# Kernel tuning notes

Measured on AMD Instinct MI355X. Metric: run time of the kernel, lower is better.

## Reference

```python
import jax, jax.numpy as jnp
import numpy as np

B, NQ, NK = 128, 64, 64
D_Q_IN = D_K_IN = D_V_IN = 1024
H, DK, DV = 16, 64, 64
D_OUT = 1024
TEMP = float(np.power(DK, 0.5))


def setup_inputs() -> dict:
    key = jax.random.key(0)
    ks = jax.random.split(key, 10)
    s = 0.01  # GroupLinearLayer init scale (0.01 * randn)
    return {
        "q": jax.random.normal(ks[0], (B, NQ, D_Q_IN), jnp.float32),
        "k": jax.random.normal(ks[1], (B, NK, D_K_IN), jnp.float32),
        "v": jax.random.normal(ks[2], (B, NK, D_V_IN), jnp.float32),
        "w_q": s * jax.random.normal(ks[3], (NQ, D_Q_IN, H * DK), jnp.float32),
        "w_k": s * jax.random.normal(ks[4], (NK, D_K_IN, H * DK), jnp.float32),
        "w_v": s * jax.random.normal(ks[5], (NK, D_V_IN, H * DV), jnp.float32),
        "fc_w": jax.random.normal(ks[6], (D_OUT, H * DV), jnp.float32) / np.sqrt(H * DV),
        "fc_b": jnp.zeros((D_OUT,), jnp.float32),
        "gate_w": jax.random.normal(ks[7], (D_OUT, H * DV), jnp.float32) / np.sqrt(H * DV),
        "gate_b": jnp.zeros((D_OUT,), jnp.float32),
    }


def reference(q, k, v, w_q, w_k, w_v, fc_w, fc_b, gate_w, gate_b):
    # Grouped (per-position) linear projections: weight [n, d_in, H*dh]
    qp = jnp.einsum('bnd,nde->bne', q, w_q).reshape(B, NQ, H, DK)
    kp = jnp.einsum('bnd,nde->bne', k, w_k).reshape(B, NK, H, DK)
    vp = jnp.einsum('bnd,nde->bne', v, w_v).reshape(B, NK, H, DV)
    # scaled dot-product attention per head
    scores = jnp.einsum('bqhd,bkhd->bhqk', qp, kp) / TEMP
    attn = jax.nn.softmax(scores, axis=-1)          # [B,H,NQ,NK]
    out = jnp.einsum('bhqk,bkhd->bqhd', attn, vp)   # [B,NQ,H,DV]
    out = out.reshape(B, NQ, H * DV)
    # fc + gated tanh output (residual=True branch; dropout p=0 -> identity)
    fc_out = out @ fc_w.T + fc_b
    gate = jax.nn.sigmoid(out @ gate_w.T + gate_b)
    output = gate * jnp.tanh(fc_out)
    return (output, attn)
```

## Files before the change

kernel.cpp:

```cpp
#include <hip/hip_runtime.h>

#define B_    128
#define NPOS  64
#define DIN   1024
#define HH    16
#define DH    64
#define E_    1024

typedef __bf16 bf16x8 __attribute__((ext_vector_type(8)));
typedef float  f32x4  __attribute__((ext_vector_type(4)));

union F4 { float4 v; float f[4]; };

__device__ __forceinline__ unsigned int pk2bf(float a, float b) {
    unsigned int ua = __float_as_uint(a);
    unsigned int ub = __float_as_uint(b);
    ua = (ua + 0x7fffu + ((ua >> 16) & 1u)) >> 16;
    ub = (ub + 0x7fffu + ((ub >> 16) & 1u)) >> 16;
    return ua | (ub << 16);
}
__device__ __forceinline__ unsigned short f2bf(float a) {
    unsigned int u = __float_as_uint(a);
    u = (u + 0x7fffu + ((u >> 16) & 1u)) >> 16;
    return (unsigned short)u;
}
__device__ __forceinline__ float bf2f(unsigned int u) {
    return __uint_as_float(u << 16);
}

__global__ __launch_bounds__(256, 3) void proj_kernel(
    const float* __restrict__ qin, const float* __restrict__ kin, const float* __restrict__ vin,
    const float* __restrict__ wq,  const float* __restrict__ wk,  const float* __restrict__ wv,
    unsigned short* __restrict__ qp, unsigned short* __restrict__ kp, unsigned short* __restrict__ vp) {
    const int e0 = blockIdx.x * 128;
    const int n  = blockIdx.y;
    const int z  = blockIdx.z;
    const float* in = (z == 0) ? qin : (z == 1) ? kin : vin;
    const float* w  = (z == 0) ? wq  : (z == 1) ? wk  : wv;
    unsigned short* outp = (z == 0) ? qp : (z == 1) ? kp : vp;

    __shared__ __attribute__((aligned(16))) unsigned short As[128 * 72];
    __shared__ __attribute__((aligned(16))) unsigned short Bs[128 * 72];

    const int t = threadIdx.x;
    const int lane = t & 63, wave = t >> 6;
    const int wm = wave >> 1, wn = wave & 1;

    f32x4 acc[4][4];
#pragma unroll
    for (int i = 0; i < 4; i++)
#pragma unroll
        for (int j = 0; j < 4; j++) acc[i][j] = (f32x4){0.f, 0.f, 0.f, 0.f};

    const float* inA = in + n * DIN;
    const float* wB  = w + (size_t)n * DIN * E_ + e0;

    const int afr = t & 15, ar0 = t >> 4;
    const int beb = t & 31, bkq = t >> 5;
    const int bS  = (beb & 7) << 4;

    F4 rA[8];
    F4 rB[2][4];

#pragma unroll
    for (int p = 0; p < 8; p++)
        rA[p].v = *(const float4*)(inA + (size_t)(ar0 + p * 16) * (NPOS * DIN) + afr * 4);
#pragma unroll
    for (int p = 0; p < 2; p++) {
        const float* src = wB + (size_t)((bkq + p * 8) * 4) * E_ + beb * 4;
#pragma unroll
        for (int x = 0; x < 4; x++) rB[p][x].v = *(const float4*)(src + (size_t)x * E_);
    }

    for (int kb = 0; kb < DIN; kb += 64) {
#pragma unroll
        for (int p = 0; p < 8; p++) {
            int row = ar0 + p * 16;
            uint2 pk; pk.x = pk2bf(rA[p].f[0], rA[p].f[1]); pk.y = pk2bf(rA[p].f[2], rA[p].f[3]);
            *(uint2*)&As[row * 72 + afr * 4] = pk;
        }
#pragma unroll
        for (int p = 0; p < 2; p++) {
            int kby = ((bkq + p * 8) * 8) ^ bS;
#pragma unroll
            for (int x = 0; x < 4; x++) {
                uint2 pk; pk.x = pk2bf(rB[p][0].f[x], rB[p][1].f[x]);
                pk.y = pk2bf(rB[p][2].f[x], rB[p][3].f[x]);
                *(uint2*)((char*)Bs + (beb * 4 + x) * 144 + kby) = pk;
            }
        }
        __syncthreads();
        if (kb + 64 < DIN) {
            const int kn = kb + 64;
#pragma unroll
            for (int p = 0; p < 8; p++)
                rA[p].v = *(const float4*)(inA + (size_t)(ar0 + p * 16) * (NPOS * DIN) + kn + afr * 4);
#pragma unroll
            for (int p = 0; p < 2; p++) {
                const float* src = wB + (size_t)(kn + (bkq + p * 8) * 4) * E_ + beb * 4;
#pragma unroll
                for (int x = 0; x < 4; x++) rB[p][x].v = *(const float4*)(src + (size_t)x * E_);
            }
        }
#pragma unroll
        for (int ks = 0; ks < 64; ks += 32) {
            bf16x8 a[4], b[4];
            const int koff = ks + (lane >> 4) * 8;
#pragma unroll
            for (int i = 0; i < 4; i++)
                a[i] = *(const bf16x8*)&As[(wm * 64 + i * 16 + (lane & 15)) * 72 + koff];
#pragma unroll
            for (int j = 0; j < 4; j++) {
                int row = wn * 64 + j * 16 + (lane & 15);
                b[j] = *(const bf16x8*)((const char*)Bs + row * 144 +
                                        ((2 * koff) ^ (((row >> 2) & 7) << 4)));
            }
#pragma unroll
            for (int i = 0; i < 4; i++)
#pragma unroll
                for (int j = 0; j < 4; j++)
                    acc[i][j] = __builtin_amdgcn_mfma_f32_16x16x32_bf16(a[i], b[j], acc[i][j], 0, 0, 0);
        }
        __syncthreads();
    }
    const int col_l = lane & 15, rq = lane >> 4;
#pragma unroll
    for (int i = 0; i < 4; i++)
#pragma unroll
        for (int j = 0; j < 4; j++) {
            int e = e0 + wn * 64 + j * 16 + col_l;
#pragma unroll
            for (int r = 0; r < 4; r++) {
                int m = wm * 64 + i * 16 + rq * 4 + r;
                outp[(size_t)m * (NPOS * E_) + n * E_ + e] = f2bf(acc[i][j][r]);
            }
        }
}

__global__ __launch_bounds__(256) void attn_kernel(
    const unsigned short* __restrict__ qp, const unsigned short* __restrict__ kp,
    const unsigned short* __restrict__ vp,
    float* __restrict__ attn_out,
    unsigned short* __restrict__ out_ws) {
    const int bid = blockIdx.x;
    const int b = bid >> 4, h = bid & 15;
    __shared__ __attribute__((aligned(16))) float qs[64 * 68];
    __shared__ __attribute__((aligned(16))) float kt[64 * 68];
    __shared__ __attribute__((aligned(16))) float sc[64 * 68];
    const int t = threadIdx.x;
    const size_t base = (size_t)b * 64 * E_ + h * DH;

#pragma unroll
    for (int p = 0; p < 4; p++) {
        int idx = p * 1024 + t * 4;
        int r = idx >> 6, c = idx & 63;
        uint2 q2 = *(const uint2*)(qp + base + r * E_ + c);
        float4 qv = { bf2f(q2.x & 0xffffu), bf2f(q2.x >> 16), bf2f(q2.y & 0xffffu), bf2f(q2.y >> 16) };
        *(float4*)&qs[r * 68 + c] = qv;
        uint2 k2 = *(const uint2*)(kp + base + r * E_ + c);
        kt[(c + 0) * 68 + r] = bf2f(k2.x & 0xffffu);
        kt[(c + 1) * 68 + r] = bf2f(k2.x >> 16);
        kt[(c + 2) * 68 + r] = bf2f(k2.y & 0xffffu);
        kt[(c + 3) * 68 + r] = bf2f(k2.y >> 16);
    }
    __syncthreads();
    const int ti = t >> 4, tj = t & 15;
    const int i0 = ti * 4, j0 = tj * 4;
    float s[4][4] = {};
    for (int k4 = 0; k4 < 64; k4 += 4) {
        F4 qv[4], kv[4];
#pragma unroll
        for (int r = 0; r < 4; r++) qv[r].v = *(const float4*)&qs[(i0 + r) * 68 + k4];
#pragma unroll
        for (int kk = 0; kk < 4; kk++) kv[kk].v = *(const float4*)&kt[(k4 + kk) * 68 + j0];
#pragma unroll
        for (int r = 0; r < 4; r++)
#pragma unroll
            for (int c = 0; c < 4; c++)
#pragma unroll
                for (int kk = 0; kk < 4; kk++)
                    s[r][c] += qv[r].f[kk] * kv[kk].f[c];
    }
#pragma unroll
    for (int r = 0; r < 4; r++)
#pragma unroll
        for (int c = 0; c < 4; c++)
            sc[(i0 + r) * 68 + j0 + c] = s[r][c] * 0.125f;
    __syncthreads();
#pragma unroll
    for (int p = 0; p < 4; p++) {
        int idx = p * 1024 + t * 4;
        int r = idx >> 6, c = idx & 63;
        uint2 v2 = *(const uint2*)(vp + base + r * E_ + c);
        float4 vv = { bf2f(v2.x & 0xffffu), bf2f(v2.x >> 16), bf2f(v2.y & 0xffffu), bf2f(v2.y >> 16) };
        *(float4*)&qs[r * 68 + c] = vv;
    }
    if (t < 64) {
        float m = -1e30f;
        for (int j = 0; j < 64; j++) m = fmaxf(m, sc[t * 68 + j]);
        float sum = 0.f;
        for (int j = 0; j < 64; j++) {
            float e = __expf(sc[t * 68 + j] - m);
            sc[t * 68 + j] = e; sum += e;
        }
        float inv = 1.f / sum;
        for (int j = 0; j < 64; j++) sc[t * 68 + j] *= inv;
    }
    __syncthreads();
    float* abase = attn_out + (size_t)bid * 4096;
#pragma unroll
    for (int p = 0; p < 4; p++) {
        int idx = p * 1024 + t * 4;
        int r = idx >> 6, c = idx & 63;
        float4 av = { sc[r * 68 + c], sc[r * 68 + c + 1], sc[r * 68 + c + 2], sc[r * 68 + c + 3] };
        *(float4*)(abase + idx) = av;
    }
    float o[4][4] = {};
    for (int j4 = 0; j4 < 64; j4 += 4) {
        F4 av[4], vv[4];
#pragma unroll
        for (int r = 0; r < 4; r++) av[r].v = *(const float4*)&sc[(i0 + r) * 68 + j4];
#pragma unroll
        for (int jj = 0; jj < 4; jj++) vv[jj].v = *(const float4*)&qs[(j4 + jj) * 68 + j0];
#pragma unroll
        for (int r = 0; r < 4; r++)
#pragma unroll
            for (int c = 0; c < 4; c++)
#pragma unroll
                for (int jj = 0; jj < 4; jj++)
                    o[r][c] += av[r].f[jj] * vv[jj].f[c];
    }
#pragma unroll
    for (int r = 0; r < 4; r++) {
        uint2 pk; pk.x = pk2bf(o[r][0], o[r][1]); pk.y = pk2bf(o[r][2], o[r][3]);
        *(uint2*)(out_ws + (size_t)(b * 64 + i0 + r) * E_ + h * DH + j0) = pk;
    }
}

__global__ __launch_bounds__(256, 2) void fcgate_kernel(
    const unsigned short* __restrict__ a,
    const float* __restrict__ fcw, const float* __restrict__ fcb,
    const float* __restrict__ gw,  const float* __restrict__ gb,
    float* __restrict__ outp) {
    const int n0 = blockIdx.x * 128;
    const int m0 = blockIdx.y * 128;
    __shared__ __attribute__((aligned(16))) unsigned short As[128 * 72];
    __shared__ __attribute__((aligned(16))) unsigned short Bf[128 * 72];
    __shared__ __attribute__((aligned(16))) unsigned short Bg[128 * 72];
    const int t = threadIdx.x;
    const int lane = t & 63, wave = t >> 6;
    const int wm = wave >> 1, wn = wave & 1;

    f32x4 accf[4][4], accg[4][4];
#pragma unroll
    for (int i = 0; i < 4; i++)
#pragma unroll
        for (int j = 0; j < 4; j++) {
            accf[i][j] = (f32x4){0.f, 0.f, 0.f, 0.f};
            accg[i][j] = (f32x4){0.f, 0.f, 0.f, 0.f};
        }

    const int afr = t & 7,  ar0 = t >> 3;
    const int bfr = t & 15, br0 = t >> 4;

    for (int kb = 0; kb < 1024; kb += 64) {
#pragma unroll
        for (int p = 0; p < 4; p++) {
            int row = ar0 + p * 32;
            *(uint4*)&As[row * 72 + afr * 8] =
                *(const uint4*)(a + (size_t)(m0 + row) * 1024 + kb + afr * 8);
        }
#pragma unroll
        for (int p = 0; p < 8; p++) {
            int row = br0 + p * 16;
            F4 cf; cf.v = *(const float4*)(fcw + (size_t)(n0 + row) * 1024 + kb + bfr * 4);
            uint2 pkf; pkf.x = pk2bf(cf.f[0], cf.f[1]); pkf.y = pk2bf(cf.f[2], cf.f[3]);
            *(uint2*)&Bf[row * 72 + bfr * 4] = pkf;
            F4 cg; cg.v = *(const float4*)(gw + (size_t)(n0 + row) * 1024 + kb + bfr * 4);
            uint2 pkg; pkg.x = pk2bf(cg.f[0], cg.f[1]); pkg.y = pk2bf(cg.f[2], cg.f[3]);
            *(uint2*)&Bg[row * 72 + bfr * 4] = pkg;
        }
        __syncthreads();
#pragma unroll
        for (int ks = 0; ks < 64; ks += 32) {
            bf16x8 av[4], bfv[4], bgv[4];
            const int koff = ks + (lane >> 4) * 8;
#pragma unroll
            for (int i = 0; i < 4; i++)
                av[i] = *(const bf16x8*)&As[(wm * 64 + i * 16 + (lane & 15)) * 72 + koff];
#pragma unroll
            for (int j = 0; j < 4; j++) {
                bfv[j] = *(const bf16x8*)&Bf[(wn * 64 + j * 16 + (lane & 15)) * 72 + koff];
                bgv[j] = *(const bf16x8*)&Bg[(wn * 64 + j * 16 + (lane & 15)) * 72 + koff];
            }
#pragma unroll
            for (int i = 0; i < 4; i++)
#pragma unroll
                for (int j = 0; j < 4; j++) {
                    accf[i][j] = __builtin_amdgcn_mfma_f32_16x16x32_bf16(av[i], bfv[j], accf[i][j], 0, 0, 0);
                    accg[i][j] = __builtin_amdgcn_mfma_f32_16x16x32_bf16(av[i], bgv[j], accg[i][j], 0, 0, 0);
                }
        }
        __syncthreads();
    }
    const int col_l = lane & 15, rq = lane >> 4;
#pragma unroll
    for (int i = 0; i < 4; i++)
#pragma unroll
        for (int j = 0; j < 4; j++) {
            int col = n0 + wn * 64 + j * 16 + col_l;
            float bfb = fcb[col], bgb = gb[col];
#pragma unroll
            for (int r = 0; r < 4; r++) {
                int m = m0 + wm * 64 + i * 16 + rq * 4 + r;
                float f = accf[i][j][r] + bfb;
                float g = accg[i][j][r] + bgb;
                float ef = __expf(2.f * f);
                float th = (ef - 1.f) / (ef + 1.f);
                float sg = 1.f / (1.f + __expf(-g));
                outp[(size_t)m * 1024 + col] = sg * th;
            }
        }
}

extern "C" void kernel_launch(void* const* d_in, const int* in_sizes, int n_in,
                              void* d_out, int out_size, void* d_ws, size_t ws_size,
                              hipStream_t stream) {
    const float* q      = (const float*)d_in[0];
    const float* k      = (const float*)d_in[1];
    const float* v      = (const float*)d_in[2];
    const float* w_q    = (const float*)d_in[3];
    const float* w_k    = (const float*)d_in[4];
    const float* w_v    = (const float*)d_in[5];
    const float* fc_w   = (const float*)d_in[6];
    const float* fc_b   = (const float*)d_in[7];
    const float* gate_w = (const float*)d_in[8];
    const float* gate_b = (const float*)d_in[9];

    float* out  = (float*)d_out;
    float* attn = out + 8388608;

    unsigned short* qp  = (unsigned short*)d_ws;
    unsigned short* kp  = qp + 8388608;
    unsigned short* vp  = kp + 8388608;
    unsigned short* ows = vp + 8388608;

    dim3 blk(256);
    proj_kernel<<<dim3(8, 64, 3), blk, 0, stream>>>(q, k, v, w_q, w_k, w_v, qp, kp, vp);
    attn_kernel<<<dim3(2048), blk, 0, stream>>>(qp, kp, vp, attn, ows);
    fcgate_kernel<<<dim3(8, 64), blk, 0, stream>>>(ows, fc_w, fc_b, gate_w, gate_b, out);
}
```

Baseline: 983.7 us.

## Rewrite attention kernel with bf16 MFMA and register-resident softmax

Replaces the scalar FP32 attention (QK^T, softmax, PV through shared-memory float tiles) with MFMA 16x16x32 bf16 instructions. Q and K fragments load straight from global memory, softmax runs in registers using lane shuffles, and V is stored transposed in swizzled LDS. The probabilities are split into hi/lo bf16 parts for two MFMAs to keep PV accuracy close to FP32. The projection kernel's B-tile swizzle pattern also changes to reduce LDS bank conflicts. The attn output is now written with scalar stores in the MFMA layout, which are less coalesced than the earlier float4 writes.

```diff
diff --git a/kernel.cpp b/kernel.cpp
--- a/kernel.cpp
+++ b/kernel.cpp
@@ -57,7 +57,7 @@
 
     const int afr = t & 15, ar0 = t >> 4;
     const int beb = t & 31, bkq = t >> 5;
-    const int bS  = (beb & 7) << 4;
+    const int bS  = ((beb >> 1) & 7) << 4;
 
     F4 rA[8];
     F4 rB[2][4];
@@ -113,7 +113,7 @@
             for (int j = 0; j < 4; j++) {
                 int row = wn * 64 + j * 16 + (lane & 15);
                 b[j] = *(const bf16x8*)((const char*)Bs + row * 144 +
-                                        ((2 * koff) ^ (((row >> 2) & 7) << 4)));
+                                        ((2 * koff) ^ (((row >> 3) & 7) << 4)));
             }
 #pragma unroll
             for (int i = 0; i < 4; i++)
@@ -144,97 +144,114 @@
     unsigned short* __restrict__ out_ws) {
     const int bid = blockIdx.x;
     const int b = bid >> 4, h = bid & 15;
-    __shared__ __attribute__((aligned(16))) float qs[64 * 68];
-    __shared__ __attribute__((aligned(16))) float kt[64 * 68];
-    __shared__ __attribute__((aligned(16))) float sc[64 * 68];
+    __shared__ __attribute__((aligned(16))) unsigned short Vt[64 * 72];
+    __shared__ __attribute__((aligned(16))) unsigned short P2[2][64 * 72];
     const int t = threadIdx.x;
-    const size_t base = (size_t)b * 64 * E_ + h * DH;
-
-#pragma unroll
-    for (int p = 0; p < 4; p++) {
-        int idx = p * 1024 + t * 4;
-        int r = idx >> 6, c = idx & 63;
-        uint2 q2 = *(const uint2*)(qp + base + r * E_ + c);
-        float4 qv = { bf2f(q2.x & 0xffffu), bf2f(q2.x >> 16), bf2f(q2.y & 0xffffu), bf2f(q2.y >> 16) };
-        *(float4*)&qs[r * 68 + c] = qv;
-        uint2 k2 = *(const uint2*)(kp + base + r * E_ + c);
-        kt[(c + 0) * 68 + r] = bf2f(k2.x & 0xffffu);
-        kt[(c + 1) * 68 + r] = bf2f(k2.x >> 16);
-        kt[(c + 2) * 68 + r] = bf2f(k2.y & 0xffffu);
-        kt[(c + 3) * 68 + r] = bf2f(k2.y >> 16);
-    }
+    const int lane = t & 63, w = t >> 6;
+    const int lr = lane & 15, lg = lane >> 4;
+    const size_t base = (size_t)b * (64 * E_) + h * DH;
+
+    const int d0 = (t & 15) * 4, j0 = (t >> 4) * 4;
+    union U2 { uint2 u; unsigned short s[4]; };
+    U2 L0, L1, L2, L3;
+    L0.u = *(const uint2*)(vp + base + (size_t)(j0 + 0) * E_ + d0);
+    L1.u = *(const uint2*)(vp + base + (size_t)(j0 + 1) * E_ + d0);
+    L2.u = *(const uint2*)(vp + base + (size_t)(j0 + 2) * E_ + d0);
+    L3.u = *(const uint2*)(vp + base + (size_t)(j0 + 3) * E_ + d0);
+
+    bf16x8 aq[2], bk[4][2];
+#pragma unroll
+    for (int ks = 0; ks < 2; ks++)
+        aq[ks] = *(const bf16x8*)(qp + base + (size_t)(w * 16 + lr) * E_ + ks * 32 + lg * 8);
+#pragma unroll
+    for (int jt = 0; jt < 4; jt++)
+#pragma unroll
+        for (int ks = 0; ks < 2; ks++)
+            bk[jt][ks] = *(const bf16x8*)(kp + base + (size_t)(jt * 16 + lr) * E_ + ks * 32 + lg * 8);
+
+#pragma unroll
+    for (int x = 0; x < 4; x++) {
+        U2 S; S.s[0] = L0.s[x]; S.s[1] = L1.s[x]; S.s[2] = L2.s[x]; S.s[3] = L3.s[x];
+        int row = d0 + x;
+        *(uint2*)((char*)Vt + row * 144 + ((j0 * 2) ^ (((row >> 3) & 7) << 4))) = S.u;
+    }
+
+    f32x4 s4[4];
+#pragma unroll
+    for (int jt = 0; jt < 4; jt++) s4[jt] = (f32x4){0.f, 0.f, 0.f, 0.f};
+#pragma unroll
+    for (int jt = 0; jt < 4; jt++)
+#pragma unroll
+        for (int ks = 0; ks < 2; ks++)
+            s4[jt] = __builtin_amdgcn_mfma_f32_16x16x32_bf16(aq[ks], bk[jt][ks], s4[jt], 0, 0, 0);
+
+    float p[4][4];
+#pragma unroll
+    for (int jt = 0; jt < 4; jt++)
+#pragma unroll
+        for (int r = 0; r < 4; r++) p[jt][r] = s4[jt][r] * 0.125f;
+
+#pragma unroll
+    for (int r = 0; r < 4; r++) {
+        float m = fmaxf(fmaxf(p[0][r], p[1][r]), fmaxf(p[2][r], p[3][r]));
+#pragma unroll
+        for (int msk = 1; msk < 16; msk <<= 1) m = fmaxf(m, __shfl_xor(m, msk));
+        float e0 = __expf(p[0][r] - m), e1 = __expf(p[1][r] - m);
+        float e2 = __expf(p[2][r] - m), e3 = __expf(p[3][r] - m);
+        float sum = (e0 + e1) + (e2 + e3);
+#pragma unroll
+        for (int msk = 1; msk < 16; msk <<= 1) sum += __shfl_xor(sum, msk);
+        float inv = 1.f / sum;
+        p[0][r] = e0 * inv; p[1][r] = e1 * inv; p[2][r] = e2 * inv; p[3][r] = e3 * inv;
+    }
+
+    float* abase = attn_out + (size_t)bid * 4096;
+#pragma unroll
+    for (int jt = 0; jt < 4; jt++)
+#pragma unroll
+        for (int r = 0; r < 4; r++) {
+            int q = w * 16 + lg * 4 + r;
+            abase[q * 64 + jt * 16 + lr] = p[jt][r];
+            unsigned short hs = f2bf(p[jt][r]);
+            float lo = p[jt][r] - bf2f(hs);
+            P2[0][q * 72 + jt * 16 + lr] = hs;
+            P2[1][q * 72 + jt * 16 + lr] = f2bf(lo);
+        }
     __syncthreads();
-    const int ti = t >> 4, tj = t & 15;
-    const int i0 = ti * 4, j0 = tj * 4;
-    float s[4][4] = {};
-    for (int k4 = 0; k4 < 64; k4 += 4) {
-        F4 qv[4], kv[4];
-#pragma unroll
-        for (int r = 0; r < 4; r++) qv[r].v = *(const float4*)&qs[(i0 + r) * 68 + k4];
-#pragma unroll
-        for (int kk = 0; kk < 4; kk++) kv[kk].v = *(const float4*)&kt[(k4 + kk) * 68 + j0];
-#pragma unroll
-        for (int r = 0; r < 4; r++)
-#pragma unroll
-            for (int c = 0; c < 4; c++)
-#pragma unroll
-                for (int kk = 0; kk < 4; kk++)
-                    s[r][c] += qv[r].f[kk] * kv[kk].f[c];
-    }
-#pragma unroll
-    for (int r = 0; r < 4; r++)
-#pragma unroll
-        for (int c = 0; c < 4; c++)
-            sc[(i0 + r) * 68 + j0 + c] = s[r][c] * 0.125f;
-    __syncthreads();
-#pragma unroll
-    for (int p = 0; p < 4; p++) {
-        int idx = p * 1024 + t * 4;
-        int r = idx >> 6, c = idx & 63;
-        uint2 v2 = *(const uint2*)(vp + base + r * E_ + c);
-        float4 vv = { bf2f(v2.x & 0xffffu), bf2f(v2.x >> 16), bf2f(v2.y & 0xffffu), bf2f(v2.y >> 16) };
-        *(float4*)&qs[r * 68 + c] = vv;
-    }
-    if (t < 64) {
-        float m = -1e30f;
-        for (int j = 0; j < 64; j++) m = fmaxf(m, sc[t * 68 + j]);
-        float sum = 0.f;
-        for (int j = 0; j < 64; j++) {
-            float e = __expf(sc[t * 68 + j] - m);
-            sc[t * 68 + j] = e; sum += e;
-        }
-        float inv = 1.f / sum;
-        for (int j = 0; j < 64; j++) sc[t * 68 + j] *= inv;
-    }
-    __syncthreads();
-    float* abase = attn_out + (size_t)bid * 4096;
-#pragma unroll
-    for (int p = 0; p < 4; p++) {
-        int idx = p * 1024 + t * 4;
-        int r = idx >> 6, c = idx & 63;
-        float4 av = { sc[r * 68 + c], sc[r * 68 + c + 1], sc[r * 68 + c + 2], sc[r * 68 + c + 3] };
-        *(float4*)(abase + idx) = av;
-    }
-    float o[4][4] = {};
-    for (int j4 = 0; j4 < 64; j4 += 4) {
-        F4 av[4], vv[4];
-#pragma unroll
-        for (int r = 0; r < 4; r++) av[r].v = *(const float4*)&sc[(i0 + r) * 68 + j4];
-#pragma unroll
-        for (int jj = 0; jj < 4; jj++) vv[jj].v = *(const float4*)&qs[(j4 + jj) * 68 + j0];
-#pragma unroll
-        for (int r = 0; r < 4; r++)
-#pragma unroll
-            for (int c = 0; c < 4; c++)
-#pragma unroll
-                for (int jj = 0; jj < 4; jj++)
-                    o[r][c] += av[r].f[jj] * vv[jj].f[c];
-    }
-#pragma unroll
-    for (int r = 0; r < 4; r++) {
-        uint2 pk; pk.x = pk2bf(o[r][0], o[r][1]); pk.y = pk2bf(o[r][2], o[r][3]);
-        *(uint2*)(out_ws + (size_t)(b * 64 + i0 + r) * E_ + h * DH + j0) = pk;
-    }
+
+    bf16x8 bv[4][2];
+#pragma unroll
+    for (int dt = 0; dt < 4; dt++)
+#pragma unroll
+        for (int ks = 0; ks < 2; ks++) {
+            int row = dt * 16 + lr;
+            bv[dt][ks] = *(const bf16x8*)((const char*)Vt + row * 144 +
+                                          ((ks * 64 + lg * 16) ^ (((row >> 3) & 7) << 4)));
+        }
+    bf16x8 ah[2], al[2];
+#pragma unroll
+    for (int ks = 0; ks < 2; ks++) {
+        ah[ks] = *(const bf16x8*)&P2[0][(w * 16 + lr) * 72 + ks * 32 + lg * 8];
+        al[ks] = *(const bf16x8*)&P2[1][(w * 16 + lr) * 72 + ks * 32 + lg * 8];
+    }
+    f32x4 o4[4];
+#pragma unroll
+    for (int dt = 0; dt < 4; dt++) o4[dt] = (f32x4){0.f, 0.f, 0.f, 0.f};
+#pragma unroll
+    for (int dt = 0; dt < 4; dt++)
+#pragma unroll
+        for (int ks = 0; ks < 2; ks++) {
+            o4[dt] = __builtin_amdgcn_mfma_f32_16x16x32_bf16(ah[ks], bv[dt][ks], o4[dt], 0, 0, 0);
+            o4[dt] = __builtin_amdgcn_mfma_f32_16x16x32_bf16(al[ks], bv[dt][ks], o4[dt], 0, 0, 0);
+        }
+
+#pragma unroll
+    for (int dt = 0; dt < 4; dt++)
+#pragma unroll
+        for (int r = 0; r < 4; r++) {
+            int q = w * 16 + lg * 4 + r;
+            out_ws[(size_t)(b * 64 + q) * E_ + h * DH + dt * 16 + lr] = f2bf(o4[dt][r]);
+        }
 }
 
 __global__ __launch_bounds__(256, 2) void fcgate_kernel(
```

Result: no change. 967.3 us (-1.7%).
